# Optimization experiments

Measured on AMD Instinct MI355X. Metric: run time of the kernel, lower is better.

The kernel has to match this reference:

```python
import jax, jax.numpy as jnp
import numpy as np

N = 8192
D_IN = 512
D_HID = 256
D_OUT = 128
NEG_SLOPE = 0.25
MASK_VAL = -1.0e12
EDGE_PROB = 0.004  # avg degree ~33


def _leaky(x):
    return jax.nn.leaky_relu(x, NEG_SLOPE)


def setup_inputs() -> dict:
    key = jax.random.key(0)
    ks = jax.random.split(key, 9)
    x = jax.random.normal(ks[0], (N, D_IN), jnp.float32)
    # sparse-ish normalized adjacency, stored dense (torch uses sparse mm / to_dense)
    vals = jax.random.uniform(ks[1], (N, N), jnp.float32)
    mask = jax.random.uniform(ks[2], (N, N)) < EDGE_PROB
    adj = jnp.where(mask, vals, 0.0).astype(jnp.float32)
    W1 = jax.random.normal(ks[3], (D_IN, D_HID), jnp.float32) * (2.0 / (D_IN + D_HID)) ** 0.5
    b1 = jnp.zeros((D_HID,), jnp.float32)
    W2 = jax.random.normal(ks[4], (D_HID, D_HID), jnp.float32) * (1.0 / D_HID) ** 0.5
    b2 = jnp.zeros((D_HID,), jnp.float32)
    Wg = jax.random.normal(ks[5], (D_HID, D_OUT), jnp.float32) * (2.0 / (D_HID + D_OUT)) ** 0.5
    a = jax.random.normal(ks[6], (2 * D_OUT, 1), jnp.float32) * 0.1
    return dict(x=x, adj=adj, W1=W1, b1=b1, W2=W2, b2=b2, Wg=Wg, a=a)


def reference(x, adj, W1, b1, W2, b2, Wg, a):
    # GCN layer 1: adj @ (x @ W1) + b1, leaky_relu (dropout p=0 / eval -> identity)
    x1 = _leaky(adj @ (x @ W1) + b1)
    # GCN layer 2
    x2 = _leaky(adj @ (x1 @ W2) + b2)
    # GAT layer: h = x2 @ Wg; e[i,j] = leaky_relu([h_i || h_j] @ a)
    # identical to leaky_relu((h@a1)_i + (h@a2)_j) without the O(N^2*2F) concat
    h = x2 @ Wg                              # [N, D_OUT]
    a1 = a[:D_OUT, 0]
    a2 = a[D_OUT:, 0]
    e = _leaky((h @ a1)[:, None] + (h @ a2)[None, :])  # [N, N]
    att = jnp.where(adj > 0, e, MASK_VAL)
    att = jax.nn.softmax(att, axis=1)
    h_prime = att @ h                        # [N, D_OUT] (concat=False -> no elu)
    out = _leaky(h_prime)
    mu = out[:, : D_OUT // 2]
    logvar = out[:, D_OUT // 2 :]
    return mu, logvar
```

## Files before the change

kernel.cpp:

```cpp
#include <hip/hip_runtime.h>

typedef unsigned short u16;
typedef u16 u16x4 __attribute__((ext_vector_type(4)));
typedef __bf16 bf16x8 __attribute__((ext_vector_type(8)));
typedef float f32x4 __attribute__((ext_vector_type(4)));

#define NROW 8192
#define CAP 128
#define D_IN 512
#define D_HID 256
#define D_OUT 128

__device__ __forceinline__ float leaky_f(float x) { return x > 0.f ? x : 0.25f * x; }

__device__ __forceinline__ u16 f2bf_rne(float f) {
  unsigned u = __float_as_uint(f);
  u += 0x7fffu + ((u >> 16) & 1u);
  return (u16)(u >> 16);
}
__device__ __forceinline__ float bf2f(u16 v) { return __uint_as_float(((unsigned)v) << 16); }
__device__ __forceinline__ void split_bf16(float f, u16& hi, u16& lo) {
  hi = f2bf_rne(f);
  float fh = __uint_as_float(((unsigned)hi) << 16);
  lo = f2bf_rne(f - fh);
}

__global__ __launch_bounds__(256) void k_packw(
    const float* __restrict__ W1, u16* __restrict__ B1,
    const float* __restrict__ W2, u16* __restrict__ B2,
    const float* __restrict__ Wg, u16* __restrict__ B3) {
  const float* W; u16* Bt; int K, Nc, idx;
  int pb = blockIdx.x;
  if (pb < 64)      { W = W1; Bt = B1; K = D_IN;  Nc = D_HID; idx = pb * 256 + threadIdx.x; }
  else if (pb < 96) { W = W2; Bt = B2; K = D_HID; Nc = D_HID; idx = (pb - 64) * 256 + threadIdx.x; }
  else              { W = Wg; Bt = B3; K = D_HID; Nc = D_OUT; idx = (pb - 96) * 256 + threadIdx.x; }
  int ko8 = K >> 3;
  int n = idx / ko8, k0 = (idx % ko8) << 3;
  alignas(16) u16 hh[8], ll[8];
#pragma unroll
  for (int j = 0; j < 8; ++j) {
    float f = W[(size_t)(k0 + j) * Nc + n];
    split_bf16(f, hh[j], ll[j]);
  }
  size_t ro = (size_t)n * 2 * K;
  *(uint4*)(Bt + ro + k0)     = *(const uint4*)hh;
  *(uint4*)(Bt + ro + K + k0) = *(const uint4*)ll;
}

__global__ __launch_bounds__(256) void k_csr_gemm1(const float* __restrict__ adj,
    int* __restrict__ cnt, int* __restrict__ cols, float* __restrict__ vals,
    const float* __restrict__ X, const u16* __restrict__ Bt, u16* __restrict__ C) {
  __shared__ u16 Ah[64 * 40], Al[64 * 40];
  __shared__ u16 Bh[64 * 40], Bl[64 * 40];
  __shared__ int csrc;
  int b = blockIdx.x;
  int tid = threadIdx.x;
  if (b < 512) {
    const int N = D_HID, K = D_IN;
    int bm = (b >> 2) * 64, bn = (b & 3) * 64;
    int wave = tid >> 6, lane = tid & 63, l15 = lane & 15, quad = lane >> 4;
    f32x4 acc[4] = {};
    int ar = tid >> 2, aj = (tid & 3) << 3;
    const float* Xrow = X + (size_t)(bm + ar) * K + aj;
    const u16* Brow = Bt + (size_t)(bn + ar) * (2 * K) + aj;
    for (int k0 = 0; k0 < K; k0 += 32) {
      alignas(16) u16 hh[8], ll[8];
      float xv[8];
      *(float4*)(xv)     = *(const float4*)(Xrow + k0);
      *(float4*)(xv + 4) = *(const float4*)(Xrow + k0 + 4);
#pragma unroll
      for (int e = 0; e < 8; ++e) split_bf16(xv[e], hh[e], ll[e]);
      *(uint4*)(&Ah[ar * 40 + aj]) = *(const uint4*)hh;
      *(uint4*)(&Al[ar * 40 + aj]) = *(const uint4*)ll;
      *(uint4*)(&Bh[ar * 40 + aj]) = *(const uint4*)(Brow + k0);
      *(uint4*)(&Bl[ar * 40 + aj]) = *(const uint4*)(Brow + K + k0);
      __syncthreads();
      bf16x8 afh = *(const bf16x8*)(&Ah[(wave * 16 + l15) * 40 + quad * 8]);
      bf16x8 afl = *(const bf16x8*)(&Al[(wave * 16 + l15) * 40 + quad * 8]);
#pragma unroll
      for (int c = 0; c < 4; ++c) {
        bf16x8 bfh = *(const bf16x8*)(&Bh[(c * 16 + l15) * 40 + quad * 8]);
        bf16x8 bfl = *(const bf16x8*)(&Bl[(c * 16 + l15) * 40 + quad * 8]);
        acc[c] = __builtin_amdgcn_mfma_f32_16x16x32_bf16(afh, bfh, acc[c], 0, 0, 0);
        acc[c] = __builtin_amdgcn_mfma_f32_16x16x32_bf16(afh, bfl, acc[c], 0, 0, 0);
        acc[c] = __builtin_amdgcn_mfma_f32_16x16x32_bf16(afl, bfh, acc[c], 0, 0, 0);
      }
      __syncthreads();
    }
#pragma unroll
    for (int c = 0; c < 4; ++c)
#pragma unroll
      for (int rg = 0; rg < 4; ++rg) {
        int rowi = bm + wave * 16 + quad * 4 + rg;
        int coli = bn + c * 16 + l15;
        C[(size_t)rowi * N + coli] = f2bf_rne(acc[c][rg]);
      }
    return;
  }
  int i = b - 512;
  if (tid == 0) csrc = 0;
  __syncthreads();
  int lane = tid & 63;
  const float4* row = (const float4*)(adj + (size_t)i * NROW);
  for (int j4 = tid; j4 < NROW / 4; j4 += 256) {
    float4 v = row[j4];
    int base = j4 * 4;
    bool p0 = v.x > 0.f, p1 = v.y > 0.f, p2 = v.z > 0.f, p3 = v.w > 0.f;
    unsigned long long m0 = __ballot(p0), m1 = __ballot(p1);
    unsigned long long m2 = __ballot(p2), m3 = __ballot(p3);
    int c0 = __popcll(m0), c1 = __popcll(m1), c2 = __popcll(m2), c3 = __popcll(m3);
    int tot = c0 + c1 + c2 + c3;
    if (tot) {
      int wbase = 0;
      if (lane == 0) wbase = atomicAdd(&csrc, tot);
      wbase = __shfl(wbase, 0);
      unsigned long long lm = (1ULL << lane) - 1ULL;
      int o0 = wbase + __popcll(m0 & lm);
      int o1 = wbase + c0 + __popcll(m1 & lm);
      int o2 = wbase + c0 + c1 + __popcll(m2 & lm);
      int o3 = wbase + c0 + c1 + c2 + __popcll(m3 & lm);
      if (p0 && o0 < CAP) { cols[i*CAP+o0] = base;   vals[i*CAP+o0] = v.x; }
      if (p1 && o1 < CAP) { cols[i*CAP+o1] = base+1; vals[i*CAP+o1] = v.y; }
      if (p2 && o2 < CAP) { cols[i*CAP+o2] = base+2; vals[i*CAP+o2] = v.z; }
      if (p3 && o3 < CAP) { cols[i*CAP+o3] = base+3; vals[i*CAP+o3] = v.w; }
    }
  }
  __syncthreads();
  if (tid == 0) cnt[i] = (csrc < CAP) ? csrc : CAP;
}

__global__ __launch_bounds__(256) void k_gemm(const u16* __restrict__ A, const u16* __restrict__ Bt,
    u16* __restrict__ C, int N, int K) {
  __shared__ u16 Ah[64 * 40], Al[64 * 40];
  __shared__ u16 Bh[64 * 40], Bl[64 * 40];
  int tid = threadIdx.x;
  int bm = blockIdx.y * 64, bn = blockIdx.x * 64;
  int wave = tid >> 6, lane = tid & 63, l15 = lane & 15, quad = lane >> 4;
  f32x4 acc[4] = {};
  int ar = tid >> 2, aj = (tid & 3) << 3;
  const u16* Arow = A + (size_t)(bm + ar) * (2 * K) + aj;
  const u16* Brow = Bt + (size_t)(bn + ar) * (2 * K) + aj;
  for (int k0 = 0; k0 < K; k0 += 32) {
    *(uint4*)(&Ah[ar * 40 + aj]) = *(const uint4*)(Arow + k0);
    *(uint4*)(&Al[ar * 40 + aj]) = *(const uint4*)(Arow + K + k0);
    *(uint4*)(&Bh[ar * 40 + aj]) = *(const uint4*)(Brow + k0);
    *(uint4*)(&Bl[ar * 40 + aj]) = *(const uint4*)(Brow + K + k0);
    __syncthreads();
    bf16x8 afh = *(const bf16x8*)(&Ah[(wave * 16 + l15) * 40 + quad * 8]);
    bf16x8 afl = *(const bf16x8*)(&Al[(wave * 16 + l15) * 40 + quad * 8]);
#pragma unroll
    for (int c = 0; c < 4; ++c) {
      bf16x8 bfh = *(const bf16x8*)(&Bh[(c * 16 + l15) * 40 + quad * 8]);
      bf16x8 bfl = *(const bf16x8*)(&Bl[(c * 16 + l15) * 40 + quad * 8]);
      acc[c] = __builtin_amdgcn_mfma_f32_16x16x32_bf16(afh, bfh, acc[c], 0, 0, 0);
      acc[c] = __builtin_amdgcn_mfma_f32_16x16x32_bf16(afh, bfl, acc[c], 0, 0, 0);
      acc[c] = __builtin_amdgcn_mfma_f32_16x16x32_bf16(afl, bfh, acc[c], 0, 0, 0);
    }
    __syncthreads();
  }
#pragma unroll
  for (int c = 0; c < 4; ++c)
#pragma unroll
    for (int rg = 0; rg < 4; ++rg) {
      int rowi = bm + wave * 16 + quad * 4 + rg;
      int coli = bn + c * 16 + l15;
      C[(size_t)rowi * N + coli] = f2bf_rne(acc[c][rg]);
    }
}

__global__ __launch_bounds__(256) void k_gemm3(const u16* __restrict__ A, const u16* __restrict__ Bt,
    u16* __restrict__ Hb, int K,
    const float* __restrict__ aptr, float* __restrict__ s1, float* __restrict__ s2) {
  __shared__ u16 Ah[32 * 40], Al[32 * 40];
  __shared__ u16 Bh[128 * 40], Bl[128 * 40];
  __shared__ float sp1[2][32], sp2[2][32];
  int tid = threadIdx.x;
  int bm = blockIdx.y * 32;
  int wave = tid >> 6, lane = tid & 63, l15 = lane & 15, quad = lane >> 4;
  int rhalf = wave >> 1, chalf = wave & 1;
  f32x4 acc[4] = {};
  int t7 = tid & 127;
  int ar = t7 >> 2, aj = (t7 & 3) << 3;
  int br = tid >> 1, bj = (tid & 1) << 4;
  const u16* Arow = A + (size_t)(bm + ar) * (2 * K) + aj + (tid < 128 ? 0 : K);
  u16* Adst = (tid < 128 ? Ah : Al) + ar * 40 + aj;
  const u16* Brow = Bt + (size_t)br * (2 * K) + bj;
  for (int k0 = 0; k0 < K; k0 += 32) {
    *(uint4*)Adst = *(const uint4*)(Arow + k0);
#pragma unroll
    for (int jj = 0; jj < 2; ++jj) {
      *(uint4*)(&Bh[br * 40 + bj + jj * 8]) = *(const uint4*)(Brow + k0 + jj * 8);
      *(uint4*)(&Bl[br * 40 + bj + jj * 8]) = *(const uint4*)(Brow + K + k0 + jj * 8);
    }
    __syncthreads();
    bf16x8 afh = *(const bf16x8*)(&Ah[(rhalf * 16 + l15) * 40 + quad * 8]);
    bf16x8 afl = *(const bf16x8*)(&Al[(rhalf * 16 + l15) * 40 + quad * 8]);
#pragma unroll
    for (int c = 0; c < 4; ++c) {
      bf16x8 bfh = *(const bf16x8*)(&Bh[(chalf * 64 + c * 16 + l15) * 40 + quad * 8]);
      bf16x8 bfl = *(const bf16x8*)(&Bl[(chalf * 64 + c * 16 + l15) * 40 + quad * 8]);
      acc[c] = __builtin_amdgcn_mfma_f32_16x16x32_bf16(afh, bfh, acc[c], 0, 0, 0);
      acc[c] = __builtin_amdgcn_mfma_f32_16x16x32_bf16(afh, bfl, acc[c], 0, 0, 0);
      acc[c] = __builtin_amdgcn_mfma_f32_16x16x32_bf16(afl, bfh, acc[c], 0, 0, 0);
    }
    __syncthreads();
  }
#pragma unroll
  for (int c = 0; c < 4; ++c)
#pragma unroll
    for (int rg = 0; rg < 4; ++rg) {
      int rowi = bm + rhalf * 16 + quad * 4 + rg;
      int coli = chalf * 64 + c * 16 + l15;
      Hb[(size_t)rowi * 128 + coli] = f2bf_rne(acc[c][rg]);
    }
  float a1v[4], a2v[4];
#pragma unroll
  for (int c = 0; c < 4; ++c) {
    a1v[c] = aptr[chalf * 64 + c * 16 + l15];
    a2v[c] = aptr[128 + chalf * 64 + c * 16 + l15];
  }
#pragma unroll
  for (int rg = 0; rg < 4; ++rg) {
    float p1 = 0.f, p2 = 0.f;
#pragma unroll
    for (int c = 0; c < 4; ++c) { p1 = fmaf(acc[c][rg], a1v[c], p1); p2 = fmaf(acc[c][rg], a2v[c], p2); }
#pragma unroll
    for (int m = 1; m < 16; m <<= 1) { p1 += __shfl_xor(p1, m); p2 += __shfl_xor(p2, m); }
    if (l15 == 0) {
      int rloc = rhalf * 16 + quad * 4 + rg;
      sp1[chalf][rloc] = p1; sp2[chalf][rloc] = p2;
    }
  }
  __syncthreads();
  if (tid < 32) {
    s1[bm + tid] = sp1[0][tid] + sp1[1][tid];
    s2[bm + tid] = sp2[0][tid] + sp2[1][tid];
  }
}

__global__ __launch_bounds__(256) void k_spmm_pack(const u16* __restrict__ Hin,
    const float* __restrict__ bias, const int* __restrict__ cnt,
    const int* __restrict__ cols, const float* __restrict__ vals, u16* __restrict__ Ap) {
  __shared__ int sc[4][CAP];
  __shared__ float sv[4][CAP];
  int w = threadIdx.x >> 6, lane = threadIdx.x & 63;
  int i = blockIdx.x * 4 + w;
  int n = cnt[i];
  if (lane < n)      { sc[w][lane]      = cols[i * CAP + lane];      sv[w][lane]      = vals[i * CAP + lane]; }
  if (lane + 64 < n) { sc[w][lane + 64] = cols[i * CAP + lane + 64]; sv[w][lane + 64] = vals[i * CAP + lane + 64]; }
  __syncthreads();
  float4 acc = {0.f, 0.f, 0.f, 0.f};
  int k = 0;
  for (; k + 7 < n; k += 8) {
    int   c0 = sc[w][k],     c1 = sc[w][k + 1], c2 = sc[w][k + 2], c3 = sc[w][k + 3];
    int   c4 = sc[w][k + 4], c5 = sc[w][k + 5], c6 = sc[w][k + 6], c7 = sc[w][k + 7];
    float w0 = sv[w][k],     w1 = sv[w][k + 1], w2 = sv[w][k + 2], w3 = sv[w][k + 3];
    float w4 = sv[w][k + 4], w5 = sv[w][k + 5], w6 = sv[w][k + 6], w7 = sv[w][k + 7];
    u16x4 v0 = *(const u16x4*)(Hin + (size_t)c0 * 256 + 4 * lane);
    u16x4 v1 = *(const u16x4*)(Hin + (size_t)c1 * 256 + 4 * lane);
    u16x4 v2 = *(const u16x4*)(Hin + (size_t)c2 * 256 + 4 * lane);
    u16x4 v3 = *(const u16x4*)(Hin + (size_t)c3 * 256 + 4 * lane);
    u16x4 v4 = *(const u16x4*)(Hin + (size_t)c4 * 256 + 4 * lane);
    u16x4 v5 = *(const u16x4*)(Hin + (size_t)c5 * 256 + 4 * lane);
    u16x4 v6 = *(const u16x4*)(Hin + (size_t)c6 * 256 + 4 * lane);
    u16x4 v7 = *(const u16x4*)(Hin + (size_t)c7 * 256 + 4 * lane);
    acc.x = fmaf(w0, bf2f(v0[0]), acc.x); acc.y = fmaf(w0, bf2f(v0[1]), acc.y);
    acc.z = fmaf(w0, bf2f(v0[2]), acc.z); acc.w = fmaf(w0, bf2f(v0[3]), acc.w);
    acc.x = fmaf(w1, bf2f(v1[0]), acc.x); acc.y = fmaf(w1, bf2f(v1[1]), acc.y);
    acc.z = fmaf(w1, bf2f(v1[2]), acc.z); acc.w = fmaf(w1, bf2f(v1[3]), acc.w);
    acc.x = fmaf(w2, bf2f(v2[0]), acc.x); acc.y = fmaf(w2, bf2f(v2[1]), acc.y);
    acc.z = fmaf(w2, bf2f(v2[2]), acc.z); acc.w = fmaf(w2, bf2f(v2[3]), acc.w);
    acc.x = fmaf(w3, bf2f(v3[0]), acc.x); acc.y = fmaf(w3, bf2f(v3[1]), acc.y);
    acc.z = fmaf(w3, bf2f(v3[2]), acc.z); acc.w = fmaf(w3, bf2f(v3[3]), acc.w);
    acc.x = fmaf(w4, bf2f(v4[0]), acc.x); acc.y = fmaf(w4, bf2f(v4[1]), acc.y);
    acc.z = fmaf(w4, bf2f(v4[2]), acc.z); acc.w = fmaf(w4, bf2f(v4[3]), acc.w);
    acc.x = fmaf(w5, bf2f(v5[0]), acc.x); acc.y = fmaf(w5, bf2f(v5[1]), acc.y);
    acc.z = fmaf(w5, bf2f(v5[2]), acc.z); acc.w = fmaf(w5, bf2f(v5[3]), acc.w);
    acc.x = fmaf(w6, bf2f(v6[0]), acc.x); acc.y = fmaf(w6, bf2f(v6[1]), acc.y);
    acc.z = fmaf(w6, bf2f(v6[2]), acc.z); acc.w = fmaf(w6, bf2f(v6[3]), acc.w);
    acc.x = fmaf(w7, bf2f(v7[0]), acc.x); acc.y = fmaf(w7, bf2f(v7[1]), acc.y);
    acc.z = fmaf(w7, bf2f(v7[2]), acc.z); acc.w = fmaf(w7, bf2f(v7[3]), acc.w);
  }
  for (; k < n; ++k) {
    float wv = sv[w][k];
    u16x4 v = *(const u16x4*)(Hin + (size_t)sc[w][k] * 256 + 4 * lane);
    acc.x = fmaf(wv, bf2f(v[0]), acc.x); acc.y = fmaf(wv, bf2f(v[1]), acc.y);
    acc.z = fmaf(wv, bf2f(v[2]), acc.z); acc.w = fmaf(wv, bf2f(v[3]), acc.w);
  }
  float4 bv = ((const float4*)bias)[lane];
  float r[4] = { leaky_f(acc.x + bv.x), leaky_f(acc.y + bv.y),
                 leaky_f(acc.z + bv.z), leaky_f(acc.w + bv.w) };
  u16x4 hi4, lo4;
#pragma unroll
  for (int e = 0; e < 4; ++e) { u16 hh, ll; split_bf16(r[e], hh, ll); hi4[e] = hh; lo4[e] = ll; }
  size_t ro = (size_t)i * 512;
  *(u16x4*)(Ap + ro + 4 * lane) = hi4;
  *(u16x4*)(Ap + ro + 256 + 4 * lane) = lo4;
}

__global__ __launch_bounds__(256) void k_attn(const u16* __restrict__ Hb,
    const float* __restrict__ s1, const float* __restrict__ s2,
    const int* __restrict__ cnt, const int* __restrict__ cols, float* __restrict__ out) {
  __shared__ int sc[4][CAP];
  __shared__ float sp[4][CAP];
  int w = threadIdx.x >> 6, lane = threadIdx.x & 63;
  int i = blockIdx.x * 4 + w;
  int n = cnt[i];
  float s1i = s1[i];
  float e0 = -1e30f, e1 = -1e30f;
  if (lane < n)      { int c = cols[i * CAP + lane];      sc[w][lane]      = c; e0 = leaky_f(s1i + s2[c]); }
  if (lane + 64 < n) { int c = cols[i * CAP + lane + 64]; sc[w][lane + 64] = c; e1 = leaky_f(s1i + s2[c]); }
  float m = fmaxf(e0, e1);
#pragma unroll
  for (int o = 32; o > 0; o >>= 1) m = fmaxf(m, __shfl_xor(m, o));
  float p0 = (lane < n)      ? expf(e0 - m) : 0.f;
  float p1 = (lane + 64 < n) ? expf(e1 - m) : 0.f;
  if (lane < n)      sp[w][lane]      = p0;
  if (lane + 64 < n) sp[w][lane + 64] = p1;
  float s = p0 + p1;
#pragma unroll
  for (int o = 32; o > 0; o >>= 1) s += __shfl_xor(s, o);
  float inv = (n > 0) ? 1.0f / s : 0.f;
  __syncthreads();
  int half = lane >> 5, t32 = lane & 31;
  float4 acc = {0.f, 0.f, 0.f, 0.f};
  int k = half;
  for (; k + 6 < n; k += 8) {
    int   c0 = sc[w][k],     c1 = sc[w][k + 2], c2 = sc[w][k + 4], c3 = sc[w][k + 6];
    float w0 = sp[w][k],     w1 = sp[w][k + 2], w2 = sp[w][k + 4], w3 = sp[w][k + 6];
    u16x4 a0 = *(const u16x4*)(Hb + (size_t)c0 * 128 + 4 * t32);
    u16x4 a1 = *(const u16x4*)(Hb + (size_t)c1 * 128 + 4 * t32);
    u16x4 a2 = *(const u16x4*)(Hb + (size_t)c2 * 128 + 4 * t32);
    u16x4 a3 = *(const u16x4*)(Hb + (size_t)c3 * 128 + 4 * t32);
    acc.x = fmaf(w0, bf2f(a0[0]), acc.x); acc.y = fmaf(w0, bf2f(a0[1]), acc.y);
    acc.z = fmaf(w0, bf2f(a0[2]), acc.z); acc.w = fmaf(w0, bf2f(a0[3]), acc.w);
    acc.x = fmaf(w1, bf2f(a1[0]), acc.x); acc.y = fmaf(w1, bf2f(a1[1]), acc.y);
    acc.z = fmaf(w1, bf2f(a1[2]), acc.z); acc.w = fmaf(w1, bf2f(a1[3]), acc.w);
    acc.x = fmaf(w2, bf2f(a2[0]), acc.x); acc.y = fmaf(w2, bf2f(a2[1]), acc.y);
    acc.z = fmaf(w2, bf2f(a2[2]), acc.z); acc.w = fmaf(w2, bf2f(a2[3]), acc.w);
    acc.x = fmaf(w3, bf2f(a3[0]), acc.x); acc.y = fmaf(w3, bf2f(a3[1]), acc.y);
    acc.z = fmaf(w3, bf2f(a3[2]), acc.z); acc.w = fmaf(w3, bf2f(a3[3]), acc.w);
  }
  for (; k < n; k += 2) {
    float wv = sp[w][k];
    u16x4 a = *(const u16x4*)(Hb + (size_t)sc[w][k] * 128 + 4 * t32);
    acc.x = fmaf(wv, bf2f(a[0]), acc.x); acc.y = fmaf(wv, bf2f(a[1]), acc.y);
    acc.z = fmaf(wv, bf2f(a[2]), acc.z); acc.w = fmaf(wv, bf2f(a[3]), acc.w);
  }
  acc.x += __shfl_xor(acc.x, 32);
  acc.y += __shfl_xor(acc.y, 32);
  acc.z += __shfl_xor(acc.z, 32);
  acc.w += __shfl_xor(acc.w, 32);
  if (lane < 32) {
    float4 r;
    r.x = leaky_f(acc.x * inv);
    r.y = leaky_f(acc.y * inv);
    r.z = leaky_f(acc.z * inv);
    r.w = leaky_f(acc.w * inv);
    float4* o4 = (float4*)out;
    if (lane < 16) o4[(size_t)i * 16 + lane] = r;
    else           o4[(size_t)NROW * 16 + (size_t)i * 16 + (lane - 16)] = r;
  }
}

extern "C" void kernel_launch(void* const* d_in, const int* in_sizes, int n_in,
                              void* d_out, int out_size, void* d_ws, size_t ws_size,
                              hipStream_t stream) {
  const float* x   = (const float*)d_in[0];
  const float* adj = (const float*)d_in[1];
  const float* W1  = (const float*)d_in[2];
  const float* b1  = (const float*)d_in[3];
  const float* W2  = (const float*)d_in[4];
  const float* b2  = (const float*)d_in[5];
  const float* Wg  = (const float*)d_in[6];
  const float* a   = (const float*)d_in[7];
  float* out = (float*)d_out;

  char* ws = (char*)d_ws;
  int*   row_cnt  = (int*)  (ws + 0);
  int*   row_cols = (int*)  (ws + 32768);
  float* row_vals = (float*)(ws + 4227072);
  u16*   B1t      = (u16*)  (ws + 8421376);
  u16*   B2t      = (u16*)  (ws + 8945664);
  u16*   B3t      = (u16*)  (ws + 9207808);
  float* s1       = (float*)(ws + 9338880);
  float* s2       = (float*)(ws + 9371648);
  u16*   hbf      = (u16*)  (ws + 9404416);
  u16*   H0T2     = (u16*)  (ws + 13598720);
  u16*   Apack    = (u16*)  (ws + 21987328);

  k_packw<<<112, 256, 0, stream>>>(W1, B1t, W2, B2t, Wg, B3t);
  k_csr_gemm1<<<512 + NROW, 256, 0, stream>>>(adj, row_cnt, row_cols, row_vals, x, B1t, H0T2);
  k_spmm_pack<<<NROW / 4, 256, 0, stream>>>(H0T2, b1, row_cnt, row_cols, row_vals, Apack);
  k_gemm<<<dim3(4, 128), 256, 0, stream>>>(Apack, B2t, H0T2, D_HID, D_HID);
  k_spmm_pack<<<NROW / 4, 256, 0, stream>>>(H0T2, b2, row_cnt, row_cols, row_vals, Apack);
  k_gemm3<<<dim3(1, 256), 256, 0, stream>>>(Apack, B3t, hbf, D_HID, a, s1, s2);
  k_attn<<<NROW / 4, 256, 0, stream>>>(hbf, s1, s2, row_cnt, row_cols, out);
}
```

Baseline: 442.7 us.

## Fuse SpMM aggregation with following dense GEMM in per-16-row blocks

Each SpMM + bias + leaky stage is merged with the dense projection that follows it, so a block of 16 rows is aggregated into LDS as split bf16 hi/lo and then multiplied by W2 or Wg with MFMA, reading B straight from global memory. This removes the packed activation round-trip through global memory and two kernel launches. The cost is lower parallelism: 512 blocks, each gathering 16 rows serially with 4 rows per wave. B fragments are also reloaded from global/L2 by every block instead of being staged in LDS.

```diff
diff --git a/kernel.cpp b/kernel.cpp
--- a/kernel.cpp
+++ b/kernel.cpp
@@ -50,8 +50,8 @@
 __global__ __launch_bounds__(256) void k_csr_gemm1(const float* __restrict__ adj,
     int* __restrict__ cnt, int* __restrict__ cols, float* __restrict__ vals,
     const float* __restrict__ X, const u16* __restrict__ Bt, u16* __restrict__ C) {
-  __shared__ u16 Ah[64 * 40], Al[64 * 40];
-  __shared__ u16 Bh[64 * 40], Bl[64 * 40];
+  __shared__ alignas(16) u16 Ah[64 * 40], Al[64 * 40];
+  __shared__ alignas(16) u16 Bh[64 * 40], Bl[64 * 40];
   __shared__ int csrc;
   int b = blockIdx.x;
   int tid = threadIdx.x;
@@ -129,133 +129,16 @@
   if (tid == 0) cnt[i] = (csrc < CAP) ? csrc : CAP;
 }
 
-__global__ __launch_bounds__(256) void k_gemm(const u16* __restrict__ A, const u16* __restrict__ Bt,
-    u16* __restrict__ C, int N, int K) {
-  __shared__ u16 Ah[64 * 40], Al[64 * 40];
-  __shared__ u16 Bh[64 * 40], Bl[64 * 40];
-  int tid = threadIdx.x;
-  int bm = blockIdx.y * 64, bn = blockIdx.x * 64;
-  int wave = tid >> 6, lane = tid & 63, l15 = lane & 15, quad = lane >> 4;
-  f32x4 acc[4] = {};
-  int ar = tid >> 2, aj = (tid & 3) << 3;
-  const u16* Arow = A + (size_t)(bm + ar) * (2 * K) + aj;
-  const u16* Brow = Bt + (size_t)(bn + ar) * (2 * K) + aj;
-  for (int k0 = 0; k0 < K; k0 += 32) {
-    *(uint4*)(&Ah[ar * 40 + aj]) = *(const uint4*)(Arow + k0);
-    *(uint4*)(&Al[ar * 40 + aj]) = *(const uint4*)(Arow + K + k0);
-    *(uint4*)(&Bh[ar * 40 + aj]) = *(const uint4*)(Brow + k0);
-    *(uint4*)(&Bl[ar * 40 + aj]) = *(const uint4*)(Brow + K + k0);
-    __syncthreads();
-    bf16x8 afh = *(const bf16x8*)(&Ah[(wave * 16 + l15) * 40 + quad * 8]);
-    bf16x8 afl = *(const bf16x8*)(&Al[(wave * 16 + l15) * 40 + quad * 8]);
-#pragma unroll
-    for (int c = 0; c < 4; ++c) {
-      bf16x8 bfh = *(const bf16x8*)(&Bh[(c * 16 + l15) * 40 + quad * 8]);
-      bf16x8 bfl = *(const bf16x8*)(&Bl[(c * 16 + l15) * 40 + quad * 8]);
-      acc[c] = __builtin_amdgcn_mfma_f32_16x16x32_bf16(afh, bfh, acc[c], 0, 0, 0);
-      acc[c] = __builtin_amdgcn_mfma_f32_16x16x32_bf16(afh, bfl, acc[c], 0, 0, 0);
-      acc[c] = __builtin_amdgcn_mfma_f32_16x16x32_bf16(afl, bfh, acc[c], 0, 0, 0);
-    }
-    __syncthreads();
-  }
-#pragma unroll
-  for (int c = 0; c < 4; ++c)
-#pragma unroll
-    for (int rg = 0; rg < 4; ++rg) {
-      int rowi = bm + wave * 16 + quad * 4 + rg;
-      int coli = bn + c * 16 + l15;
-      C[(size_t)rowi * N + coli] = f2bf_rne(acc[c][rg]);
-    }
-}
-
-__global__ __launch_bounds__(256) void k_gemm3(const u16* __restrict__ A, const u16* __restrict__ Bt,
-    u16* __restrict__ Hb, int K,
-    const float* __restrict__ aptr, float* __restrict__ s1, float* __restrict__ s2) {
-  __shared__ u16 Ah[32 * 40], Al[32 * 40];
-  __shared__ u16 Bh[128 * 40], Bl[128 * 40];
-  __shared__ float sp1[2][32], sp2[2][32];
-  int tid = threadIdx.x;
-  int bm = blockIdx.y * 32;
-  int wave = tid >> 6, lane = tid & 63, l15 = lane & 15, quad = lane >> 4;
-  int rhalf = wave >> 1, chalf = wave & 1;
-  f32x4 acc[4] = {};
-  int t7 = tid & 127;
-  int ar = t7 >> 2, aj = (t7 & 3) << 3;
-  int br = tid >> 1, bj = (tid & 1) << 4;
-  const u16* Arow = A + (size_t)(bm + ar) * (2 * K) + aj + (tid < 128 ? 0 : K);
-  u16* Adst = (tid < 128 ? Ah : Al) + ar * 40 + aj;
-  const u16* Brow = Bt + (size_t)br * (2 * K) + bj;
-  for (int k0 = 0; k0 < K; k0 += 32) {
-    *(uint4*)Adst = *(const uint4*)(Arow + k0);
-#pragma unroll
-    for (int jj = 0; jj < 2; ++jj) {
-      *(uint4*)(&Bh[br * 40 + bj + jj * 8]) = *(const uint4*)(Brow + k0 + jj * 8);
-      *(uint4*)(&Bl[br * 40 + bj + jj * 8]) = *(const uint4*)(Brow + K + k0 + jj * 8);
-    }
-    __syncthreads();
-    bf16x8 afh = *(const bf16x8*)(&Ah[(rhalf * 16 + l15) * 40 + quad * 8]);
-    bf16x8 afl = *(const bf16x8*)(&Al[(rhalf * 16 + l15) * 40 + quad * 8]);
-#pragma unroll
-    for (int c = 0; c < 4; ++c) {
-      bf16x8 bfh = *(const bf16x8*)(&Bh[(chalf * 64 + c * 16 + l15) * 40 + quad * 8]);
-      bf16x8 bfl = *(const bf16x8*)(&Bl[(chalf * 64 + c * 16 + l15) * 40 + quad * 8]);
-      acc[c] = __builtin_amdgcn_mfma_f32_16x16x32_bf16(afh, bfh, acc[c], 0, 0, 0);
-      acc[c] = __builtin_amdgcn_mfma_f32_16x16x32_bf16(afh, bfl, acc[c], 0, 0, 0);
-      acc[c] = __builtin_amdgcn_mfma_f32_16x16x32_bf16(afl, bfh, acc[c], 0, 0, 0);
-    }
-    __syncthreads();
-  }
-#pragma unroll
-  for (int c = 0; c < 4; ++c)
-#pragma unroll
-    for (int rg = 0; rg < 4; ++rg) {
-      int rowi = bm + rhalf * 16 + quad * 4 + rg;
-      int coli = chalf * 64 + c * 16 + l15;
-      Hb[(size_t)rowi * 128 + coli] = f2bf_rne(acc[c][rg]);
-    }
-  float a1v[4], a2v[4];
-#pragma unroll
-  for (int c = 0; c < 4; ++c) {
-    a1v[c] = aptr[chalf * 64 + c * 16 + l15];
-    a2v[c] = aptr[128 + chalf * 64 + c * 16 + l15];
-  }
-#pragma unroll
-  for (int rg = 0; rg < 4; ++rg) {
-    float p1 = 0.f, p2 = 0.f;
-#pragma unroll
-    for (int c = 0; c < 4; ++c) { p1 = fmaf(acc[c][rg], a1v[c], p1); p2 = fmaf(acc[c][rg], a2v[c], p2); }
-#pragma unroll
-    for (int m = 1; m < 16; m <<= 1) { p1 += __shfl_xor(p1, m); p2 += __shfl_xor(p2, m); }
-    if (l15 == 0) {
-      int rloc = rhalf * 16 + quad * 4 + rg;
-      sp1[chalf][rloc] = p1; sp2[chalf][rloc] = p2;
-    }
-  }
-  __syncthreads();
-  if (tid < 32) {
-    s1[bm + tid] = sp1[0][tid] + sp1[1][tid];
-    s2[bm + tid] = sp2[0][tid] + sp2[1][tid];
-  }
-}
-
-__global__ __launch_bounds__(256) void k_spmm_pack(const u16* __restrict__ Hin,
-    const float* __restrict__ bias, const int* __restrict__ cnt,
-    const int* __restrict__ cols, const float* __restrict__ vals, u16* __restrict__ Ap) {
-  __shared__ int sc[4][CAP];
-  __shared__ float sv[4][CAP];
-  int w = threadIdx.x >> 6, lane = threadIdx.x & 63;
-  int i = blockIdx.x * 4 + w;
-  int n = cnt[i];
-  if (lane < n)      { sc[w][lane]      = cols[i * CAP + lane];      sv[w][lane]      = vals[i * CAP + lane]; }
-  if (lane + 64 < n) { sc[w][lane + 64] = cols[i * CAP + lane + 64]; sv[w][lane + 64] = vals[i * CAP + lane + 64]; }
-  __syncthreads();
+
+__device__ __forceinline__ float4 gather_row256(const u16* __restrict__ Hin,
+    const int* scw, const float* svw, int n, int lane) {
   float4 acc = {0.f, 0.f, 0.f, 0.f};
   int k = 0;
   for (; k + 7 < n; k += 8) {
-    int   c0 = sc[w][k],     c1 = sc[w][k + 1], c2 = sc[w][k + 2], c3 = sc[w][k + 3];
-    int   c4 = sc[w][k + 4], c5 = sc[w][k + 5], c6 = sc[w][k + 6], c7 = sc[w][k + 7];
-    float w0 = sv[w][k],     w1 = sv[w][k + 1], w2 = sv[w][k + 2], w3 = sv[w][k + 3];
-    float w4 = sv[w][k + 4], w5 = sv[w][k + 5], w6 = sv[w][k + 6], w7 = sv[w][k + 7];
+    int   c0 = scw[k],     c1 = scw[k + 1], c2 = scw[k + 2], c3 = scw[k + 3];
+    int   c4 = scw[k + 4], c5 = scw[k + 5], c6 = scw[k + 6], c7 = scw[k + 7];
+    float w0 = svw[k],     w1 = svw[k + 1], w2 = svw[k + 2], w3 = svw[k + 3];
+    float w4 = svw[k + 4], w5 = svw[k + 5], w6 = svw[k + 6], w7 = svw[k + 7];
     u16x4 v0 = *(const u16x4*)(Hin + (size_t)c0 * 256 + 4 * lane);
     u16x4 v1 = *(const u16x4*)(Hin + (size_t)c1 * 256 + 4 * lane);
     u16x4 v2 = *(const u16x4*)(Hin + (size_t)c2 * 256 + 4 * lane);
@@ -282,20 +165,154 @@
     acc.z = fmaf(w7, bf2f(v7[2]), acc.z); acc.w = fmaf(w7, bf2f(v7[3]), acc.w);
   }
   for (; k < n; ++k) {
-    float wv = sv[w][k];
-    u16x4 v = *(const u16x4*)(Hin + (size_t)sc[w][k] * 256 + 4 * lane);
+    float wv = svw[k];
+    u16x4 v = *(const u16x4*)(Hin + (size_t)scw[k] * 256 + 4 * lane);
     acc.x = fmaf(wv, bf2f(v[0]), acc.x); acc.y = fmaf(wv, bf2f(v[1]), acc.y);
     acc.z = fmaf(wv, bf2f(v[2]), acc.z); acc.w = fmaf(wv, bf2f(v[3]), acc.w);
   }
+  return acc;
+}
+
+__global__ __launch_bounds__(256) void k_fuse1(const u16* __restrict__ Hin,
+    const float* __restrict__ bias, const int* __restrict__ cnt,
+    const int* __restrict__ cols, const float* __restrict__ vals,
+    const u16* __restrict__ Bt, u16* __restrict__ Cout) {
+  __shared__ alignas(16) u16 AhF[8 * 16 * 40], AlF[8 * 16 * 40];
+  __shared__ int   sc[4 * CAP];
+  __shared__ float sv[4 * CAP];
+  int tid = threadIdx.x;
+  int wave = tid >> 6, lane = tid & 63, l15 = lane & 15, quad = lane >> 4;
+  int bm = blockIdx.x * 16;
+  int* scw = sc + wave * CAP;
+  float* svw = sv + wave * CAP;
   float4 bv = ((const float4*)bias)[lane];
-  float r[4] = { leaky_f(acc.x + bv.x), leaky_f(acc.y + bv.y),
-                 leaky_f(acc.z + bv.z), leaky_f(acc.w + bv.w) };
-  u16x4 hi4, lo4;
-#pragma unroll
-  for (int e = 0; e < 4; ++e) { u16 hh, ll; split_bf16(r[e], hh, ll); hi4[e] = hh; lo4[e] = ll; }
-  size_t ro = (size_t)i * 512;
-  *(u16x4*)(Ap + ro + 4 * lane) = hi4;
-  *(u16x4*)(Ap + ro + 256 + 4 * lane) = lo4;
+#pragma unroll
+  for (int rr = 0; rr < 4; ++rr) {
+    int r = wave * 4 + rr;
+    int i = bm + r;
+    int n = cnt[i];
+    if (lane < n)      { scw[lane]      = cols[i*CAP+lane];      svw[lane]      = vals[i*CAP+lane]; }
+    if (lane + 64 < n) { scw[lane + 64] = cols[i*CAP+lane+64];   svw[lane + 64] = vals[i*CAP+lane+64]; }
+    float4 acc = gather_row256(Hin, scw, svw, n, lane);
+    float r4[4] = { leaky_f(acc.x + bv.x), leaky_f(acc.y + bv.y),
+                    leaky_f(acc.z + bv.z), leaky_f(acc.w + bv.w) };
+    u16x4 hi4, lo4;
+#pragma unroll
+    for (int e = 0; e < 4; ++e) { u16 hh, ll; split_bf16(r4[e], hh, ll); hi4[e] = hh; lo4[e] = ll; }
+    int dst = (lane >> 3) * 640 + r * 40 + (lane & 7) * 4;
+    *(u16x4*)(&AhF[dst]) = hi4;
+    *(u16x4*)(&AlF[dst]) = lo4;
+  }
+  __syncthreads();
+#pragma unroll
+  for (int hN = 0; hN < 2; ++hN) {
+    f32x4 acc[2] = {};
+#pragma unroll
+    for (int k0 = 0; k0 < D_HID; k0 += 32) {
+      bf16x8 afh = *(const bf16x8*)(&AhF[(k0 >> 5) * 640 + l15 * 40 + quad * 8]);
+      bf16x8 afl = *(const bf16x8*)(&AlF[(k0 >> 5) * 640 + l15 * 40 + quad * 8]);
+#pragma unroll
+      for (int c = 0; c < 2; ++c) {
+        int col = hN * 128 + wave * 32 + c * 16 + l15;
+        const u16* bp = Bt + (size_t)col * (2 * D_HID) + k0 + quad * 8;
+        bf16x8 bfh = *(const bf16x8*)(bp);
+        bf16x8 bfl = *(const bf16x8*)(bp + D_HID);
+        acc[c] = __builtin_amdgcn_mfma_f32_16x16x32_bf16(afh, bfh, acc[c], 0, 0, 0);
+        acc[c] = __builtin_amdgcn_mfma_f32_16x16x32_bf16(afh, bfl, acc[c], 0, 0, 0);
+        acc[c] = __builtin_amdgcn_mfma_f32_16x16x32_bf16(afl, bfh, acc[c], 0, 0, 0);
+      }
+    }
+#pragma unroll
+    for (int c = 0; c < 2; ++c)
+#pragma unroll
+      for (int rg = 0; rg < 4; ++rg) {
+        int rowi = bm + quad * 4 + rg;
+        int coli = hN * 128 + wave * 32 + c * 16 + l15;
+        Cout[(size_t)rowi * 256 + coli] = f2bf_rne(acc[c][rg]);
+      }
+  }
+}
+
+__global__ __launch_bounds__(256) void k_fuse2(const u16* __restrict__ Hin,
+    const float* __restrict__ bias, const int* __restrict__ cnt,
+    const int* __restrict__ cols, const float* __restrict__ vals,
+    const u16* __restrict__ Bt, u16* __restrict__ Hb,
+    const float* __restrict__ aptr, float* __restrict__ s1, float* __restrict__ s2) {
+  __shared__ alignas(16) u16 AhF[8 * 16 * 40], AlF[8 * 16 * 40];
+  __shared__ int   sc[4 * CAP];
+  __shared__ float sv[4 * CAP];
+  __shared__ float sp1[4][16], sp2[4][16];
+  int tid = threadIdx.x;
+  int wave = tid >> 6, lane = tid & 63, l15 = lane & 15, quad = lane >> 4;
+  int bm = blockIdx.x * 16;
+  int* scw = sc + wave * CAP;
+  float* svw = sv + wave * CAP;
+  float4 bv = ((const float4*)bias)[lane];
+#pragma unroll
+  for (int rr = 0; rr < 4; ++rr) {
+    int r = wave * 4 + rr;
+    int i = bm + r;
+    int n = cnt[i];
+    if (lane < n)      { scw[lane]      = cols[i*CAP+lane];      svw[lane]      = vals[i*CAP+lane]; }
+    if (lane + 64 < n) { scw[lane + 64] = cols[i*CAP+lane+64];   svw[lane + 64] = vals[i*CAP+lane+64]; }
+    float4 acc = gather_row256(Hin, scw, svw, n, lane);
+    float r4[4] = { leaky_f(acc.x + bv.x), leaky_f(acc.y + bv.y),
+                    leaky_f(acc.z + bv.z), leaky_f(acc.w + bv.w) };
+    u16x4 hi4, lo4;
+#pragma unroll
+    for (int e = 0; e < 4; ++e) { u16 hh, ll; split_bf16(r4[e], hh, ll); hi4[e] = hh; lo4[e] = ll; }
+    int dst = (lane >> 3) * 640 + r * 40 + (lane & 7) * 4;
+    *(u16x4*)(&AhF[dst]) = hi4;
+    *(u16x4*)(&AlF[dst]) = lo4;
+  }
+  __syncthreads();
+  f32x4 acc[2] = {};
+#pragma unroll
+  for (int k0 = 0; k0 < D_HID; k0 += 32) {
+    bf16x8 afh = *(const bf16x8*)(&AhF[(k0 >> 5) * 640 + l15 * 40 + quad * 8]);
+    bf16x8 afl = *(const bf16x8*)(&AlF[(k0 >> 5) * 640 + l15 * 40 + quad * 8]);
+#pragma unroll
+    for (int c = 0; c < 2; ++c) {
+      int col = wave * 32 + c * 16 + l15;
+      const u16* bp = Bt + (size_t)col * (2 * D_HID) + k0 + quad * 8;
+      bf16x8 bfh = *(const bf16x8*)(bp);
+      bf16x8 bfl = *(const bf16x8*)(bp + D_HID);
+      acc[c] = __builtin_amdgcn_mfma_f32_16x16x32_bf16(afh, bfh, acc[c], 0, 0, 0);
+      acc[c] = __builtin_amdgcn_mfma_f32_16x16x32_bf16(afh, bfl, acc[c], 0, 0, 0);
+      acc[c] = __builtin_amdgcn_mfma_f32_16x16x32_bf16(afl, bfh, acc[c], 0, 0, 0);
+    }
+  }
+#pragma unroll
+  for (int c = 0; c < 2; ++c)
+#pragma unroll
+    for (int rg = 0; rg < 4; ++rg) {
+      int rowi = bm + quad * 4 + rg;
+      int coli = wave * 32 + c * 16 + l15;
+      Hb[(size_t)rowi * 128 + coli] = f2bf_rne(acc[c][rg]);
+    }
+  float a1v[2], a2v[2];
+#pragma unroll
+  for (int c = 0; c < 2; ++c) {
+    a1v[c] = aptr[wave * 32 + c * 16 + l15];
+    a2v[c] = aptr[128 + wave * 32 + c * 16 + l15];
+  }
+#pragma unroll
+  for (int rg = 0; rg < 4; ++rg) {
+    float p1 = 0.f, p2 = 0.f;
+#pragma unroll
+    for (int c = 0; c < 2; ++c) { p1 = fmaf(acc[c][rg], a1v[c], p1); p2 = fmaf(acc[c][rg], a2v[c], p2); }
+#pragma unroll
+    for (int m = 1; m < 16; m <<= 1) { p1 += __shfl_xor(p1, m); p2 += __shfl_xor(p2, m); }
+    if (l15 == 0) {
+      int rloc = quad * 4 + rg;
+      sp1[wave][rloc] = p1; sp2[wave][rloc] = p2;
+    }
+  }
+  __syncthreads();
+  if (tid < 16) {
+    s1[bm + tid] = sp1[0][tid] + sp1[1][tid] + sp1[2][tid] + sp1[3][tid];
+    s2[bm + tid] = sp2[0][tid] + sp2[1][tid] + sp2[2][tid] + sp2[3][tid];
+  }
 }
 
 __global__ __launch_bounds__(256) void k_attn(const u16* __restrict__ Hb,
@@ -387,13 +404,11 @@
   float* s2       = (float*)(ws + 9371648);
   u16*   hbf      = (u16*)  (ws + 9404416);
   u16*   H0T2     = (u16*)  (ws + 13598720);
-  u16*   Apack    = (u16*)  (ws + 21987328);
+  u16*   T2       = (u16*)  (ws + 21987328);
 
   k_packw<<<112, 256, 0, stream>>>(W1, B1t, W2, B2t, Wg, B3t);
   k_csr_gemm1<<<512 + NROW, 256, 0, stream>>>(adj, row_cnt, row_cols, row_vals, x, B1t, H0T2);
-  k_spmm_pack<<<NROW / 4, 256, 0, stream>>>(H0T2, b1, row_cnt, row_cols, row_vals, Apack);
-  k_gemm<<<dim3(4, 128), 256, 0, stream>>>(Apack, B2t, H0T2, D_HID, D_HID);
-  k_spmm_pack<<<NROW / 4, 256, 0, stream>>>(H0T2, b2, row_cnt, row_cols, row_vals, Apack);
-  k_gemm3<<<dim3(1, 256), 256, 0, stream>>>(Apack, B3t, hbf, D_HID, a, s1, s2);
+  k_fuse1<<<NROW / 16, 256, 0, stream>>>(H0T2, b1, row_cnt, row_cols, row_vals, B2t, T2);
+  k_fuse2<<<NROW / 16, 256, 0, stream>>>(T2, b2, row_cnt, row_cols, row_vals, B3t, hbf, a, s1, s2);
   k_attn<<<NROW / 4, 256, 0, stream>>>(hbf, s1, s2, row_cnt, row_cols, out);
 }
```

Measured after the change: 447.3 us. Within noise of the previous version (+1.0%).
